# Kernel optimization log

Measured on AMD Instinct MI355X. Metric: run time of the kernel, lower is better.

## Reference

```python
import jax, jax.numpy as jnp
import numpy as np

H = 4          # num_attention_heads
DH = 32        # attention_head_size
C = H * DH     # all_head_size = 128
WS = 7         # window side -> dim = 49
DIM = WS * WS
B = 4096       # number of windows
TABLE = (2 * WS - 1) ** 2  # 169


def setup_inputs() -> dict:
    key = jax.random.key(0)
    ks = jax.random.split(key, 10)
    s = 0.02
    return {
        "hidden_states": jax.random.normal(ks[0], (B, DIM, C), jnp.float32),
        "attention_mask": jax.random.normal(ks[1], (B, DIM, DIM), jnp.float32),
        "Wq": jax.random.normal(ks[2], (C, C), jnp.float32) * s,
        "bq": jax.random.normal(ks[3], (C,), jnp.float32) * s,
        "Wk": jax.random.normal(ks[4], (C, C), jnp.float32) * s,
        "bk": jax.random.normal(ks[5], (C,), jnp.float32) * s,
        "Wv": jax.random.normal(ks[6], (C, C), jnp.float32) * s,
        "bv": jax.random.normal(ks[7], (C,), jnp.float32) * s,
        "relative_position_bias_table": jax.random.normal(ks[8], (TABLE, H), jnp.float32) * s,
        "relative_position_index": jax.random.randint(ks[9], (DIM * DIM,), 0, TABLE, jnp.int64),
    }


def reference(hidden_states, attention_mask, Wq, bq, Wk, bk, Wv, bv,
              relative_position_bias_table, relative_position_index):
    b, n, _ = hidden_states.shape
    # QKV projections -> [b, H, n, DH]
    def proj(W, bias):
        y = jnp.einsum('bnc,cd->bnd', hidden_states, W.T) + bias
        return y.reshape(b, n, H, DH).transpose(0, 2, 1, 3)
    q = proj(Wq, bq)
    k = proj(Wk, bk)
    v = proj(Wv, bv)
    scores = jnp.einsum('bhnd,bhmd->bhnm', q, k) / jnp.sqrt(jnp.float32(DH))
    # relative position bias gather: [n*n] -> [n, n, H] -> [H, n, n]
    bias = relative_position_bias_table[relative_position_index].reshape(n, n, H)
    bias = bias.transpose(2, 0, 1)
    scores = scores + bias[None] + attention_mask[:, None]
    probs = jax.nn.softmax(scores, axis=-1)
    ctx = jnp.einsum('bhnm,bhmd->bhnd', probs, v)
    ctx = ctx.transpose(0, 2, 1, 3).reshape(b, n, H * DH)
    return ctx
```

## Files before the change

kernel.cpp:

```cpp
#include <hip/hip_runtime.h>
#include <hip/hip_bf16.h>


#define SEQ 49
#define CH 128
#define NH 4
#define DHD 32
#define NTAB 169

typedef __hip_bfloat16 bf16;
typedef __attribute__((ext_vector_type(8))) short bf16x8;
typedef __attribute__((ext_vector_type(4))) float f32x4;

#define WP_FRAGS (3*NH*2*4*64)
#define WP_BYTES (WP_FRAGS*8*2)
#define BIAS_ELEMS (NH*64*64)
#define BIAS_BYTES (BIAS_ELEMS*4)
#define WS_NEED ((size_t)(WP_BYTES + BIAS_BYTES))

__device__ __forceinline__ bf16x8 pack8(float4 a, float4 b) {
    alignas(16) bf16 t[8] = {
        __float2bfloat16(a.x), __float2bfloat16(a.y),
        __float2bfloat16(a.z), __float2bfloat16(a.w),
        __float2bfloat16(b.x), __float2bfloat16(b.y),
        __float2bfloat16(b.z), __float2bfloat16(b.w)};
    return *(const bf16x8*)t;
}

__device__ __forceinline__ unsigned pk2(float lo, float hi) {
    union { bf16 h[2]; unsigned u; } r;
    r.h[0] = __float2bfloat16(lo);
    r.h[1] = __float2bfloat16(hi);
    return r.u;
}

__device__ __forceinline__ bf16x8 regroup(unsigned pk0_0, unsigned pk0_1,
                                          unsigned pk1_0, unsigned pk1_1,
                                          int srcA, int srcB, bool hiT) {
    union { unsigned u[4]; bf16x8 v; } o;
    unsigned a0 = (unsigned)__shfl((int)pk0_0, srcA);
    unsigned b0 = (unsigned)__shfl((int)pk1_0, srcA);
    unsigned a1 = (unsigned)__shfl((int)pk0_1, srcA);
    unsigned b1 = (unsigned)__shfl((int)pk1_1, srcA);
    unsigned a2 = (unsigned)__shfl((int)pk0_0, srcB);
    unsigned b2 = (unsigned)__shfl((int)pk1_0, srcB);
    unsigned a3 = (unsigned)__shfl((int)pk0_1, srcB);
    unsigned b3 = (unsigned)__shfl((int)pk1_1, srcB);
    o.u[0] = hiT ? b0 : a0;
    o.u[1] = hiT ? b1 : a1;
    o.u[2] = hiT ? b2 : a2;
    o.u[3] = hiT ? b3 : a3;
    return o.v;
}

__global__ void prep_kernel(const float* __restrict__ Wq,
                            const float* __restrict__ Wk,
                            const float* __restrict__ Wv,
                            const float* __restrict__ table,
                            const int*  __restrict__ ridx,
                            bf16* __restrict__ wp,
                            float* __restrict__ bias_t) {
    int i = blockIdx.x*256 + threadIdx.x;
    if (i < WP_FRAGS) {
        int lane = i & 63, ks = (i >> 6) & 3, t = (i >> 8) & 1;
        int h = (i >> 9) & 3, which = i >> 11;
        const float* W = which == 0 ? Wq : (which == 1 ? Wk : Wv);
        const float* p = W + (h*DHD + t*16 + (lane & 15))*CH + ks*32 + (lane >> 4)*8;
        ((bf16x8*)wp)[i] = pack8(*(const float4*)p, *(const float4*)(p + 4));
    } else {
        int j = i - WP_FRAGS;
        if (j < BIAS_ELEMS) {
            int h = j >> 12, n = (j >> 6) & 63, m = j & 63;
            float v = 0.f;
            if (n < SEQ && m < SEQ) {
                int idx = ridx[m*SEQ + n];
                idx = idx < 0 ? 0 : (idx > NTAB-1 ? NTAB-1 : idx);
                v = table[idx*NH + h];
            }
            bias_t[j] = v;
        }
    }
}

template<bool WS>
__global__ __launch_bounds__(64, 4) void swin_attn_kernel(
    const float* __restrict__ hs,
    const float* __restrict__ amask,
    const float* __restrict__ Wq, const float* __restrict__ bq,
    const float* __restrict__ Wk, const float* __restrict__ bk,
    const float* __restrict__ Wv, const float* __restrict__ bv,
    const float* __restrict__ table,
    const int*  __restrict__ ridx,
    const bf16*  __restrict__ wp,
    const float* __restrict__ bias_t,
    float* __restrict__ out)
{
    const int b = blockIdx.x >> 2;
    const int h = blockIdx.x & 3;
    const int lane = threadIdx.x & 63;
    const int l = lane & 15;
    const int q = lane >> 4;
    const int srcA = ((q & 1) << 5) | l;
    const int srcB = srcA + 16;
    const bool hiT = q >= 2;

    const float* xb = hs + (size_t)b*SEQ*CH;
    const f32x4 z4 = {0.f, 0.f, 0.f, 0.f};

    auto loadX = [&](int rt, int ks) -> bf16x8 {
        int row = rt*16 + l; row = row > SEQ-1 ? SEQ-1 : row;
        const float* p = xb + row*CH + ks*32 + q*8;
        return pack8(*(const float4*)p, *(const float4*)(p + 4));
    };
    auto loadW = [&](int which, int t, int ks) -> bf16x8 {
        if (WS) {
            return *(const bf16x8*)(wp +
                ((((size_t)(which*NH + h)*2 + t)*4 + ks)*64 + lane)*8);
        } else {
            const float* W = which == 0 ? Wq : (which == 1 ? Wk : Wv);
            const float* p = W + (h*DHD + t*16 + l)*CH + ks*32 + q*8;
            return pack8(*(const float4*)p, *(const float4*)(p + 4));
        }
    };

    bf16x8 fQ[4], fK[4];
#pragma unroll
    for (int which = 0; which < 2; ++which) {
        f32x4 acc[2][4] = {{z4,z4,z4,z4},{z4,z4,z4,z4}};
#pragma unroll
        for (int ks = 0; ks < 4; ++ks) {
            bf16x8 xf[4];
#pragma unroll
            for (int rt = 0; rt < 4; ++rt) xf[rt] = loadX(rt, ks);
#pragma unroll
            for (int t = 0; t < 2; ++t) {
                const bf16x8 wf = loadW(which, t, ks);
#pragma unroll
                for (int rt = 0; rt < 4; ++rt)
                    acc[t][rt] = __builtin_amdgcn_mfma_f32_16x16x32_bf16(
                        wf, xf[rt], acc[t][rt], 0, 0, 0);
            }
        }
        const float* bvec = which == 0 ? bq : bk;
        unsigned pk[2][4][2];
#pragma unroll
        for (int t = 0; t < 2; ++t) {
            const float b0 = bvec[h*DHD + t*16 + 4*q + 0];
            const float b1 = bvec[h*DHD + t*16 + 4*q + 1];
            const float b2 = bvec[h*DHD + t*16 + 4*q + 2];
            const float b3 = bvec[h*DHD + t*16 + 4*q + 3];
#pragma unroll
            for (int rt = 0; rt < 4; ++rt) {
                pk[t][rt][0] = pk2(acc[t][rt][0] + b0, acc[t][rt][1] + b1);
                pk[t][rt][1] = pk2(acc[t][rt][2] + b2, acc[t][rt][3] + b3);
            }
        }
#pragma unroll
        for (int rt = 0; rt < 4; ++rt) {
            const bf16x8 f = regroup(pk[0][rt][0], pk[0][rt][1],
                                     pk[1][rt][0], pk[1][rt][1], srcA, srcB, hiT);
            if (which == 0) fQ[rt] = f; else fK[rt] = f;
        }
    }

    f32x4 accV[4][2] = {{z4,z4},{z4,z4},{z4,z4},{z4,z4}};
#pragma unroll
    for (int ks = 0; ks < 4; ++ks) {
        bf16x8 xf[4];
#pragma unroll
        for (int nt = 0; nt < 4; ++nt) xf[nt] = loadX(nt, ks);
#pragma unroll
        for (int dt = 0; dt < 2; ++dt) {
            const bf16x8 wf = loadW(2, dt, ks);
#pragma unroll
            for (int nt = 0; nt < 4; ++nt)
                accV[nt][dt] = __builtin_amdgcn_mfma_f32_16x16x32_bf16(
                    xf[nt], wf, accV[nt][dt], 0, 0, 0);
        }
    }
    unsigned pkv[4][2][2];
#pragma unroll
    for (int nt = 0; nt < 4; ++nt)
#pragma unroll
        for (int dt = 0; dt < 2; ++dt) {
            pkv[nt][dt][0] = pk2(accV[nt][dt][0], accV[nt][dt][1]);
            pkv[nt][dt][1] = pk2(accV[nt][dt][2], accV[nt][dt][3]);
        }
    bf16x8 fV[2][2];
#pragma unroll
    for (int dt = 0; dt < 2; ++dt)
#pragma unroll
        for (int ks2 = 0; ks2 < 2; ++ks2)
            fV[dt][ks2] = regroup(pkv[2*ks2][dt][0],   pkv[2*ks2][dt][1],
                                  pkv[2*ks2+1][dt][0], pkv[2*ks2+1][dt][1],
                                  srcA, srcB, hiT);

    f32x4 S[4][4];
#pragma unroll
    for (int kt = 0; kt < 4; ++kt)
#pragma unroll
        for (int qt = 0; qt < 4; ++qt)
            S[kt][qt] = __builtin_amdgcn_mfma_f32_16x16x32_bf16(
                fK[kt], fQ[qt], z4, 0, 0, 0);

    const float scale = 0.17677669529663687f;
    const float* maskb = amask + (size_t)b*SEQ*SEQ;
    const float* biash = WS ? bias_t + h*4096 : nullptr;
    unsigned pkp[4][4][2];
#pragma unroll
    for (int qt = 0; qt < 4; ++qt) {
        const int m = qt*16 + l;
        const int mc = m > SEQ-1 ? SEQ-1 : m;
        float mx = -3.0e38f;
#pragma unroll
        for (int kt = 0; kt < 4; ++kt)
#pragma unroll
            for (int r = 0; r < 4; ++r) {
                const int n = kt*16 + 4*q + r;
                const int nc = n > SEQ-1 ? SEQ-1 : n;
                float bt;
                if (WS) {
                    bt = biash[n*64 + m];
                } else {
                    int idx = ridx[mc*SEQ + nc];
                    idx = idx < 0 ? 0 : (idx > NTAB-1 ? NTAB-1 : idx);
                    bt = table[idx*NH + h];
                }
                const float mk = maskb[mc*SEQ + nc];
                const float s = (n < SEQ) ? S[kt][qt][r]*scale + bt + mk
                                          : -30000.f;
                S[kt][qt][r] = s;
                mx = fmaxf(mx, s);
            }
        mx = fmaxf(mx, __shfl_xor(mx, 16));
        mx = fmaxf(mx, __shfl_xor(mx, 32));
        float sum = 0.f;
#pragma unroll
        for (int kt = 0; kt < 4; ++kt)
#pragma unroll
            for (int r = 0; r < 4; ++r) {
                const float e = __expf(S[kt][qt][r] - mx);
                S[kt][qt][r] = e;
                sum += e;
            }
        sum += __shfl_xor(sum, 16);
        sum += __shfl_xor(sum, 32);
        const float inv = 1.f / sum;
#pragma unroll
        for (int kt = 0; kt < 4; ++kt) {
            pkp[kt][qt][0] = pk2(S[kt][qt][0]*inv, S[kt][qt][1]*inv);
            pkp[kt][qt][1] = pk2(S[kt][qt][2]*inv, S[kt][qt][3]*inv);
        }
    }

    f32x4 O[4][2] = {{z4,z4},{z4,z4},{z4,z4},{z4,z4}};
#pragma unroll
    for (int qt = 0; qt < 4; ++qt)
#pragma unroll
        for (int ks2 = 0; ks2 < 2; ++ks2) {
            const bf16x8 ap = regroup(pkp[2*ks2][qt][0],   pkp[2*ks2][qt][1],
                                      pkp[2*ks2+1][qt][0], pkp[2*ks2+1][qt][1],
                                      srcA, srcB, hiT);
#pragma unroll
            for (int dt = 0; dt < 2; ++dt)
                O[qt][dt] = __builtin_amdgcn_mfma_f32_16x16x32_bf16(
                    ap, fV[dt][ks2], O[qt][dt], 0, 0, 0);
        }

    const float bv0 = bv[h*DHD + l];
    const float bv1 = bv[h*DHD + 16 + l];
    float* ob = out + (size_t)b*SEQ*CH + h*DHD;
#pragma unroll
    for (int qt = 0; qt < 4; ++qt)
#pragma unroll
        for (int r = 0; r < 4; ++r) {
            const int m = qt*16 + 4*q + r;
            if (m < SEQ) {
                ob[m*CH + l]      = O[qt][0][r] + bv0;
                ob[m*CH + 16 + l] = O[qt][1][r] + bv1;
            }
        }
}

extern "C" void kernel_launch(void* const* d_in, const int* in_sizes, int n_in,
                              void* d_out, int out_size, void* d_ws, size_t ws_size,
                              hipStream_t stream) {
    (void)n_in; (void)out_size;
    const int nwin = in_sizes[0] / (SEQ * CH);
    const bool usews = (d_ws != nullptr) && (ws_size >= WS_NEED);
    if (usews) {
        bf16* wp = (bf16*)d_ws;
        float* bias_t = (float*)((char*)d_ws + WP_BYTES);
        prep_kernel<<<dim3((WP_FRAGS + BIAS_ELEMS + 255)/256), dim3(256), 0, stream>>>(
            (const float*)d_in[2], (const float*)d_in[4], (const float*)d_in[6],
            (const float*)d_in[8], (const int*)d_in[9], wp, bias_t);
        swin_attn_kernel<true><<<dim3(nwin*NH), dim3(64), 0, stream>>>(
            (const float*)d_in[0], (const float*)d_in[1],
            (const float*)d_in[2], (const float*)d_in[3],
            (const float*)d_in[4], (const float*)d_in[5],
            (const float*)d_in[6], (const float*)d_in[7],
            (const float*)d_in[8], (const int*)d_in[9],
            wp, bias_t, (float*)d_out);
    } else {
        swin_attn_kernel<false><<<dim3(nwin*NH), dim3(64), 0, stream>>>(
            (const float*)d_in[0], (const float*)d_in[1],
            (const float*)d_in[2], (const float*)d_in[3],
            (const float*)d_in[4], (const float*)d_in[5],
            (const float*)d_in[6], (const float*)d_in[7],
            (const float*)d_in[8], (const int*)d_in[9],
            nullptr, nullptr, (float*)d_out);
    }
}
```

Baseline: 358.6 us.

## Drop cross-lane regroup shuffles, fold scale into Q, one block per window

Removes the shuffle-based regroup of MFMA outputs by feeding accumulator registers straight into the next MFMA's operand slots, which relies on a consistent k-index permutation between operands. Folds the softmax scale into Q before bf16 packing, and moves the V projection after the softmax. Launches one 256-thread block per window with one wave per head instead of one 64-thread block per head, so the four heads share X loads through cache. Adds s_setprio around the MFMA bursts. The permutation trick must keep the contraction consistent, and the 256-thread launch bound changes the register budget.

```diff
diff --git a/kernel.cpp b/kernel.cpp
--- a/kernel.cpp
+++ b/kernel.cpp
@@ -34,24 +34,7 @@
     return r.u;
 }
 
-__device__ __forceinline__ bf16x8 regroup(unsigned pk0_0, unsigned pk0_1,
-                                          unsigned pk1_0, unsigned pk1_1,
-                                          int srcA, int srcB, bool hiT) {
-    union { unsigned u[4]; bf16x8 v; } o;
-    unsigned a0 = (unsigned)__shfl((int)pk0_0, srcA);
-    unsigned b0 = (unsigned)__shfl((int)pk1_0, srcA);
-    unsigned a1 = (unsigned)__shfl((int)pk0_1, srcA);
-    unsigned b1 = (unsigned)__shfl((int)pk1_1, srcA);
-    unsigned a2 = (unsigned)__shfl((int)pk0_0, srcB);
-    unsigned b2 = (unsigned)__shfl((int)pk1_0, srcB);
-    unsigned a3 = (unsigned)__shfl((int)pk0_1, srcB);
-    unsigned b3 = (unsigned)__shfl((int)pk1_1, srcB);
-    o.u[0] = hiT ? b0 : a0;
-    o.u[1] = hiT ? b1 : a1;
-    o.u[2] = hiT ? b2 : a2;
-    o.u[3] = hiT ? b3 : a3;
-    return o.v;
-}
+union frag_u { unsigned u[4]; bf16x8 v; };
 
 __global__ void prep_kernel(const float* __restrict__ Wq,
                             const float* __restrict__ Wk,
@@ -83,7 +66,7 @@
 }
 
 template<bool WS>
-__global__ __launch_bounds__(64, 4) void swin_attn_kernel(
+__global__ __launch_bounds__(256, 4) void swin_attn_kernel(
     const float* __restrict__ hs,
     const float* __restrict__ amask,
     const float* __restrict__ Wq, const float* __restrict__ bq,
@@ -95,14 +78,11 @@
     const float* __restrict__ bias_t,
     float* __restrict__ out)
 {
-    const int b = blockIdx.x >> 2;
-    const int h = blockIdx.x & 3;
+    const int b = blockIdx.x;
+    const int h = threadIdx.x >> 6;
     const int lane = threadIdx.x & 63;
     const int l = lane & 15;
     const int q = lane >> 4;
-    const int srcA = ((q & 1) << 5) | l;
-    const int srcB = srcA + 16;
-    const bool hiT = q >= 2;
 
     const float* xb = hs + (size_t)b*SEQ*CH;
     const f32x4 z4 = {0.f, 0.f, 0.f, 0.f};
@@ -142,68 +122,34 @@
             }
         }
         const float* bvec = which == 0 ? bq : bk;
-        unsigned pk[2][4][2];
-#pragma unroll
-        for (int t = 0; t < 2; ++t) {
-            const float b0 = bvec[h*DHD + t*16 + 4*q + 0];
-            const float b1 = bvec[h*DHD + t*16 + 4*q + 1];
-            const float b2 = bvec[h*DHD + t*16 + 4*q + 2];
-            const float b3 = bvec[h*DHD + t*16 + 4*q + 3];
-#pragma unroll
-            for (int rt = 0; rt < 4; ++rt) {
-                pk[t][rt][0] = pk2(acc[t][rt][0] + b0, acc[t][rt][1] + b1);
-                pk[t][rt][1] = pk2(acc[t][rt][2] + b2, acc[t][rt][3] + b3);
-            }
-        }
+        const float sc = which == 0 ? 0.17677669529663687f : 1.0f;
+        float bb[2][4];
+#pragma unroll
+        for (int t = 0; t < 2; ++t)
+#pragma unroll
+            for (int r = 0; r < 4; ++r)
+                bb[t][r] = bvec[h*DHD + t*16 + 4*q + r];
 #pragma unroll
         for (int rt = 0; rt < 4; ++rt) {
-            const bf16x8 f = regroup(pk[0][rt][0], pk[0][rt][1],
-                                     pk[1][rt][0], pk[1][rt][1], srcA, srcB, hiT);
-            if (which == 0) fQ[rt] = f; else fK[rt] = f;
-        }
-    }
-
-    f32x4 accV[4][2] = {{z4,z4},{z4,z4},{z4,z4},{z4,z4}};
-#pragma unroll
-    for (int ks = 0; ks < 4; ++ks) {
-        bf16x8 xf[4];
-#pragma unroll
-        for (int nt = 0; nt < 4; ++nt) xf[nt] = loadX(nt, ks);
-#pragma unroll
-        for (int dt = 0; dt < 2; ++dt) {
-            const bf16x8 wf = loadW(2, dt, ks);
-#pragma unroll
-            for (int nt = 0; nt < 4; ++nt)
-                accV[nt][dt] = __builtin_amdgcn_mfma_f32_16x16x32_bf16(
-                    xf[nt], wf, accV[nt][dt], 0, 0, 0);
-        }
-    }
-    unsigned pkv[4][2][2];
-#pragma unroll
-    for (int nt = 0; nt < 4; ++nt)
-#pragma unroll
-        for (int dt = 0; dt < 2; ++dt) {
-            pkv[nt][dt][0] = pk2(accV[nt][dt][0], accV[nt][dt][1]);
-            pkv[nt][dt][1] = pk2(accV[nt][dt][2], accV[nt][dt][3]);
-        }
-    bf16x8 fV[2][2];
-#pragma unroll
-    for (int dt = 0; dt < 2; ++dt)
-#pragma unroll
-        for (int ks2 = 0; ks2 < 2; ++ks2)
-            fV[dt][ks2] = regroup(pkv[2*ks2][dt][0],   pkv[2*ks2][dt][1],
-                                  pkv[2*ks2+1][dt][0], pkv[2*ks2+1][dt][1],
-                                  srcA, srcB, hiT);
+            frag_u f;
+            f.u[0] = pk2((acc[0][rt][0]+bb[0][0])*sc, (acc[0][rt][1]+bb[0][1])*sc);
+            f.u[1] = pk2((acc[0][rt][2]+bb[0][2])*sc, (acc[0][rt][3]+bb[0][3])*sc);
+            f.u[2] = pk2((acc[1][rt][0]+bb[1][0])*sc, (acc[1][rt][1]+bb[1][1])*sc);
+            f.u[3] = pk2((acc[1][rt][2]+bb[1][2])*sc, (acc[1][rt][3]+bb[1][3])*sc);
+            if (which == 0) fQ[rt] = f.v; else fK[rt] = f.v;
+        }
+    }
 
     f32x4 S[4][4];
+    __builtin_amdgcn_s_setprio(1);
 #pragma unroll
     for (int kt = 0; kt < 4; ++kt)
 #pragma unroll
         for (int qt = 0; qt < 4; ++qt)
             S[kt][qt] = __builtin_amdgcn_mfma_f32_16x16x32_bf16(
                 fK[kt], fQ[qt], z4, 0, 0, 0);
-
-    const float scale = 0.17677669529663687f;
+    __builtin_amdgcn_s_setprio(0);
+
     const float* maskb = amask + (size_t)b*SEQ*SEQ;
     const float* biash = WS ? bias_t + h*4096 : nullptr;
     unsigned pkp[4][4][2];
@@ -211,6 +157,7 @@
     for (int qt = 0; qt < 4; ++qt) {
         const int m = qt*16 + l;
         const int mc = m > SEQ-1 ? SEQ-1 : m;
+        const float* mrow = maskb + (size_t)mc*SEQ;
         float mx = -3.0e38f;
 #pragma unroll
         for (int kt = 0; kt < 4; ++kt)
@@ -226,8 +173,7 @@
                     idx = idx < 0 ? 0 : (idx > NTAB-1 ? NTAB-1 : idx);
                     bt = table[idx*NH + h];
                 }
-                const float mk = maskb[mc*SEQ + nc];
-                const float s = (n < SEQ) ? S[kt][qt][r]*scale + bt + mk
+                const float s = (n < SEQ) ? S[kt][qt][r] + bt + mrow[nc]
                                           : -30000.f;
                 S[kt][qt][r] = s;
                 mx = fmaxf(mx, s);
@@ -253,19 +199,51 @@
         }
     }
 
+    f32x4 accV[4][2] = {{z4,z4},{z4,z4},{z4,z4},{z4,z4}};
+#pragma unroll
+    for (int ks = 0; ks < 4; ++ks) {
+        bf16x8 xf[4];
+#pragma unroll
+        for (int nt = 0; nt < 4; ++nt) xf[nt] = loadX(nt, ks);
+#pragma unroll
+        for (int dt = 0; dt < 2; ++dt) {
+            const bf16x8 wf = loadW(2, dt, ks);
+#pragma unroll
+            for (int nt = 0; nt < 4; ++nt)
+                accV[nt][dt] = __builtin_amdgcn_mfma_f32_16x16x32_bf16(
+                    xf[nt], wf, accV[nt][dt], 0, 0, 0);
+        }
+    }
+    bf16x8 fV[2][2];
+#pragma unroll
+    for (int dt = 0; dt < 2; ++dt)
+#pragma unroll
+        for (int ks2 = 0; ks2 < 2; ++ks2) {
+            frag_u f;
+            f.u[0] = pk2(accV[2*ks2][dt][0],   accV[2*ks2][dt][1]);
+            f.u[1] = pk2(accV[2*ks2][dt][2],   accV[2*ks2][dt][3]);
+            f.u[2] = pk2(accV[2*ks2+1][dt][0], accV[2*ks2+1][dt][1]);
+            f.u[3] = pk2(accV[2*ks2+1][dt][2], accV[2*ks2+1][dt][3]);
+            fV[dt][ks2] = f.v;
+        }
+
     f32x4 O[4][2] = {{z4,z4},{z4,z4},{z4,z4},{z4,z4}};
+    __builtin_amdgcn_s_setprio(1);
 #pragma unroll
     for (int qt = 0; qt < 4; ++qt)
 #pragma unroll
         for (int ks2 = 0; ks2 < 2; ++ks2) {
-            const bf16x8 ap = regroup(pkp[2*ks2][qt][0],   pkp[2*ks2][qt][1],
-                                      pkp[2*ks2+1][qt][0], pkp[2*ks2+1][qt][1],
-                                      srcA, srcB, hiT);
+            frag_u a;
+            a.u[0] = pkp[2*ks2][qt][0];
+            a.u[1] = pkp[2*ks2][qt][1];
+            a.u[2] = pkp[2*ks2+1][qt][0];
+            a.u[3] = pkp[2*ks2+1][qt][1];
 #pragma unroll
             for (int dt = 0; dt < 2; ++dt)
                 O[qt][dt] = __builtin_amdgcn_mfma_f32_16x16x32_bf16(
-                    ap, fV[dt][ks2], O[qt][dt], 0, 0, 0);
-        }
+                    a.v, fV[dt][ks2], O[qt][dt], 0, 0, 0);
+        }
+    __builtin_amdgcn_s_setprio(0);
 
     const float bv0 = bv[h*DHD + l];
     const float bv1 = bv[h*DHD + 16 + l];
@@ -294,7 +272,7 @@
         prep_kernel<<<dim3((WP_FRAGS + BIAS_ELEMS + 255)/256), dim3(256), 0, stream>>>(
             (const float*)d_in[2], (const float*)d_in[4], (const float*)d_in[6],
             (const float*)d_in[8], (const int*)d_in[9], wp, bias_t);
-        swin_attn_kernel<true><<<dim3(nwin*NH), dim3(64), 0, stream>>>(
+        swin_attn_kernel<true><<<dim3(nwin), dim3(256), 0, stream>>>(
             (const float*)d_in[0], (const float*)d_in[1],
             (const float*)d_in[2], (const float*)d_in[3],
             (const float*)d_in[4], (const float*)d_in[5],
@@ -302,7 +280,7 @@
             (const float*)d_in[8], (const int*)d_in[9],
             wp, bias_t, (float*)d_out);
     } else {
-        swin_attn_kernel<false><<<dim3(nwin*NH), dim3(64), 0, stream>>>(
+        swin_attn_kernel<false><<<dim3(nwin), dim3(256), 0, stream>>>(
             (const float*)d_in[0], (const float*)d_in[1],
             (const float*)d_in[2], (const float*)d_in[3],
             (const float*)d_in[4], (const float*)d_in[5],
```

Result: slower. 389.7 us (+8.7%).
